# Kernel tuning notes

Hardware: AMD Instinct MI355X
Metric: run time of the kernel (lower is better)

Reference implementation:

```python
import jax, jax.numpy as jnp
import numpy as np

H_IN, W_IN = 128, 128  # sensor grid; region=(1,1), stride=(1,1) -> one RF per pixel


def setup_inputs() -> dict:
    key = jax.random.key(0)
    k1, k2, k3, k4, k5, k6 = jax.random.split(key, 6)
    B, N, C, HID = 8, 2048, 16, 128
    s = 1.0 / np.sqrt(HID)
    features = jax.random.normal(k1, (B, N, C), dtype=jnp.float32)
    coords = jax.random.randint(k2, (B, N, 2), 0, 128, dtype=jnp.int32)  # (x, y)
    w_ih = jax.random.normal(k3, (4 * HID, C), dtype=jnp.float32) * s
    w_hh = jax.random.normal(k4, (4 * HID, HID), dtype=jnp.float32) * s
    b_ih = jax.random.normal(k5, (4 * HID,), dtype=jnp.float32) * s
    b_hh = jax.random.normal(k6, (4 * HID,), dtype=jnp.float32) * s
    return {"features": features, "coords": coords, "w_ih": w_ih,
            "w_hh": w_hh, "b_ih": b_ih, "b_hh": b_hh}


def reference(features, coords, w_ih, w_hh, b_ih, b_hh):
    """MatrixLSTM with 1x1 non-overlapping receptive fields.

    Events (time-ordered along axis 1) are routed to their pixel's RF; a shared
    LSTM is run over each RF's event sequence and the last output per RF is
    scattered into a dense [B, hidden, H, W] map (zeros where no events).
    Implemented as one lax.scan over events with per-RF (h, c) state.
    """
    B, N, C = features.shape
    HID = w_hh.shape[1]
    # coord2idx: raster order y * W + x  -> RF id per event, [B, N]
    rf = coords[:, :, 1].astype(jnp.int32) * W_IN + coords[:, :, 0].astype(jnp.int32)
    bidx = jnp.arange(B)
    bias = b_ih + b_hh

    def step(carry, inp):
        h_all, c_all = carry              # [B, num_rf, HID] each
        x_t, rf_t = inp                   # [B, C], [B]
        h_prev = h_all[bidx, rf_t]        # gather per-RF state, [B, HID]
        c_prev = c_all[bidx, rf_t]
        gates = x_t @ w_ih.T + h_prev @ w_hh.T + bias  # [B, 4*HID]
        i, f, g, o = jnp.split(gates, 4, axis=-1)       # torch LSTM gate order
        i = jax.nn.sigmoid(i)
        f = jax.nn.sigmoid(f)
        g = jnp.tanh(g)
        o = jax.nn.sigmoid(o)
        c_new = f * c_prev + i * g
        h_new = o * jnp.tanh(c_new)
        h_all = h_all.at[bidx, rf_t].set(h_new)        # scatter back
        c_all = c_all.at[bidx, rf_t].set(c_new)
        return (h_all, c_all), None

    h0 = jnp.zeros((B, H_IN * W_IN, HID), features.dtype)
    c0 = jnp.zeros_like(h0)
    (h_all, _), _ = jax.lax.scan(step, (h0, c0),
                                 (features.transpose(1, 0, 2), rf.T))
    # final h per RF == LSTM output at each RF's last event; zeros if no events
    return h_all.reshape(B, H_IN, W_IN, HID).transpose(0, 3, 1, 2)
```

## Files before the change

kernel.cpp:

```cpp
#include <hip/hip_runtime.h>
#include <hip/hip_bf16.h>
#include <math.h>

#define B 8
#define N 2048
#define C 16
#define HID 128
#define NRF 16384
#define MAXLEN 8
#define MAXCH 2048

__device__ __forceinline__ float sigf(float x) { return 1.f / (1.f + expf(-x)); }

__global__ __launch_bounds__(1024) void k_pre(
    const int* __restrict__ coords, const float* __restrict__ w_ih,
    const float* __restrict__ w_hh, const float* __restrict__ b_ih,
    const float* __restrict__ b_hh, float* __restrict__ w_ih_T,
    float* __restrict__ w_hh_T, float* __restrict__ biassum,
    int* __restrict__ map, int* __restrict__ cnt, int* __restrict__ chainrf,
    int* __restrict__ chainlen, int* __restrict__ slots,
    int* __restrict__ m2cnt, int* __restrict__ mlist2) {
    int tid = threadIdx.x;
    if (blockIdx.x < 8) {
        int bb = blockIdx.x;
        __shared__ int cnt_l[NRF];
        __shared__ int nch_l, nmul_l;
#pragma unroll
        for (int i = 0; i < 16; i++) cnt_l[tid + 1024 * i] = 0;
        if (tid == 0) { nch_l = 0; nmul_l = 0; }
#pragma unroll
        for (int i = 0; i < 16; i++) map[bb * NRF + tid + 1024 * i] = -1;
        __syncthreads();
        int n0 = tid, n1 = tid + 1024;
        int2 c0 = ((const int2*)coords)[bb * N + n0];
        int2 c1 = ((const int2*)coords)[bb * N + n1];
        int rf0 = c0.y * 128 + c0.x;
        int rf1 = c1.y * 128 + c1.x;
        int pos0 = atomicAdd(&cnt_l[rf0], 1);
        int pos1 = atomicAdd(&cnt_l[rf1], 1);
        if (pos0 < MAXLEN) slots[((size_t)bb * NRF + rf0) * MAXLEN + pos0] = n0;
        if (pos1 < MAXLEN) slots[((size_t)bb * NRF + rf1) * MAXLEN + pos1] = n1;
        __syncthreads();
#pragma unroll
        for (int e = 0; e < 2; e++) {
            int rf = e ? rf1 : rf0;
            int pos = e ? pos1 : pos0;
            if (pos == 0) {
                int j = atomicAdd(&nch_l, 1);
                int len = cnt_l[rf];
                if (len > MAXLEN) len = MAXLEN;
                chainrf[bb * MAXCH + j] = rf;
                chainlen[bb * MAXCH + j] = len;
                map[bb * NRF + rf] = j;
                if (len >= 2) {
                    int m = atomicAdd(&nmul_l, 1);
                    if (m < 256) mlist2[bb * 256 + m] = bb * MAXCH + j;
                }
            }
        }
        __syncthreads();
        if (tid == 0) {
            cnt[bb] = nch_l;
            m2cnt[bb * 16] = (nmul_l > 256) ? 256 : nmul_l;
        }
    } else {
        int i = (blockIdx.x - 8) * 1024 + tid;
        if (i < C * 512) {
            int c = i >> 9, j = i & 511;
            w_ih_T[i] = w_ih[j * C + c];
        }
        if (i < HID * 512) {
            int k = i >> 9, j = i & 511;
            w_hh_T[i] = w_hh[j * HID + k];
        }
        if (i < 512) biassum[i] = b_ih[i] + b_hh[i];
    }
}

__global__ __launch_bounds__(256) void k_phase0(
    const float* __restrict__ features, const float* __restrict__ w_ih_T,
    const float* __restrict__ biassum, const int* __restrict__ cnt,
    const int* __restrict__ chainrf, const int* __restrict__ chainlen,
    int* __restrict__ slots, float* __restrict__ hfin,
    float* __restrict__ cfin) {
    int tid = threadIdx.x;
    int bb = blockIdx.x >> 8;
    int slot0 = (blockIdx.x & 255) * 8;
    __shared__ float ls_w[C * 512];
    __shared__ float ls_b[512];
    __shared__ int l_idx[8], l_len[8], l_ev0[8];
    int nc = cnt[bb];
    if (tid < 8) {
        int j = slot0 + tid;
        int idx = bb * MAXCH + j;
        if (j < nc) {
            int len = chainlen[idx];
            int* sl = slots + ((size_t)bb * NRF + chainrf[idx]) * MAXLEN;
            int ev0;
            if (len >= 2) {
                int ev[MAXLEN];
#pragma unroll
                for (int t = 0; t < MAXLEN; t++) {
                    int v = sl[t];
                    ev[t] = (t < len) ? v : 0x7fffffff;
                }
#pragma unroll
                for (int a = 0; a < MAXLEN; a++)
#pragma unroll
                    for (int q = 0; q < MAXLEN - 1; q++) {
                        int u = ev[q], v = ev[q + 1];
                        ev[q] = min(u, v);
                        ev[q + 1] = max(u, v);
                    }
                for (int t = 0; t < len; t++) sl[t] = ev[t];
                ev0 = ev[0];
            } else {
                ev0 = sl[0];
            }
            l_idx[tid] = idx; l_len[tid] = len; l_ev0[tid] = ev0;
        } else {
            l_idx[tid] = -1;
        }
    }
    for (int i = tid; i < C * 512; i += 256) ls_w[i] = w_ih_T[i];
    ls_b[tid] = biassum[tid];
    ls_b[tid + 256] = biassum[tid + 256];
    __syncthreads();
    int w = tid >> 6, lane = tid & 63;
#pragma unroll
    for (int s2 = 0; s2 < 2; s2++) {
        int s = 2 * w + s2;
        int idx = l_idx[s];
        if (idx < 0) continue;
        int len = l_len[s];
        int n = l_ev0[s];
        float f = 0.f;
        if (lane < 16) f = features[((size_t)(bb * N + n)) * C + lane];
        float ai0 = ls_b[lane],       ai1 = ls_b[lane + 64];
        float ag0 = ls_b[lane + 256], ag1 = ls_b[lane + 320];
        float ao0 = ls_b[lane + 384], ao1 = ls_b[lane + 448];
#pragma unroll
        for (int c2 = 0; c2 < 16; c2++) {
            float xv = __shfl(f, c2, 64);
            ai0 += ls_w[c2 * 512 + lane]       * xv;
            ai1 += ls_w[c2 * 512 + lane + 64]  * xv;
            ag0 += ls_w[c2 * 512 + lane + 256] * xv;
            ag1 += ls_w[c2 * 512 + lane + 320] * xv;
            ao0 += ls_w[c2 * 512 + lane + 384] * xv;
            ao1 += ls_w[c2 * 512 + lane + 448] * xv;
        }
        float c0 = sigf(ai0) * tanhf(ag0);
        float c1 = sigf(ai1) * tanhf(ag1);
        float h0 = sigf(ao0) * tanhf(c0);
        float h1 = sigf(ao1) * tanhf(c1);
        hfin[(size_t)idx * HID + lane] = h0;
        hfin[(size_t)idx * HID + lane + 64] = h1;
        if (len >= 2) {
            cfin[(size_t)idx * HID + lane] = c0;
            cfin[(size_t)idx * HID + lane + 64] = c1;
        }
    }
}

__global__ __launch_bounds__(512) void k_recur(
    const float* __restrict__ features, const float* __restrict__ w_ih_T,
    const float* __restrict__ w_hh_T, const float* __restrict__ biassum,
    const int* __restrict__ chainrf, const int* __restrict__ chainlen,
    const int* __restrict__ slots, const int* __restrict__ m2cnt,
    const int* __restrict__ mlist2, float* __restrict__ hfin,
    const float* __restrict__ cfin) {
    int tid = threadIdx.x;
    int bb = blockIdx.x >> 7;
    int j0 = blockIdx.x & 127;
    int Mb = m2cnt[bb * 16];
    if (j0 >= Mb) return;
    __shared__ float h_s[HID];
    __shared__ float x_s[16];
    __shared__ float g_s[512];
    float wi[16];
#pragma unroll
    for (int c2 = 0; c2 < 16; c2++) wi[c2] = w_ih_T[c2 * 512 + tid];
    float bsum = biassum[tid];
    for (int j = j0; j < Mb; j += 128) {
        int idx = mlist2[bb * 256 + j];
        int len = chainlen[idx];
        const int* sl = slots + ((size_t)bb * NRF + chainrf[idx]) * MAXLEN;
        if (tid < 128) h_s[tid] = hfin[(size_t)idx * HID + tid];
        float c = (tid < 128) ? cfin[(size_t)idx * HID + tid] : 0.f;
        __syncthreads();
        for (int t = 1; t < len; t++) {
            int n = sl[t];
            if (tid < 16) x_s[tid] = features[((size_t)(bb * N + n)) * C + tid];
            __syncthreads();
            float a0 = bsum, a1 = 0.f, a2 = 0.f, a3 = 0.f;
#pragma unroll
            for (int c2 = 0; c2 < 16; c2++) a0 += wi[c2] * x_s[c2];
#pragma unroll 8
            for (int k = 0; k < 128; k += 4) {
                a0 += w_hh_T[k * 512 + tid] * h_s[k];
                a1 += w_hh_T[(k + 1) * 512 + tid] * h_s[k + 1];
                a2 += w_hh_T[(k + 2) * 512 + tid] * h_s[k + 2];
                a3 += w_hh_T[(k + 3) * 512 + tid] * h_s[k + 3];
            }
            g_s[tid] = (a0 + a1) + (a2 + a3);
            __syncthreads();
            if (tid < 128) {
                float ig = sigf(g_s[tid]);
                float fg = sigf(g_s[tid + 128]);
                float gg = tanhf(g_s[tid + 256]);
                float og = sigf(g_s[tid + 384]);
                c = fg * c + ig * gg;
                h_s[tid] = og * tanhf(c);
            }
            __syncthreads();
        }
        if (tid < 128) hfin[(size_t)idx * HID + tid] = h_s[tid];
        __syncthreads();
    }
}

__global__ __launch_bounds__(256) void k_scatter(
    const float* __restrict__ hfin, const int* __restrict__ map,
    float* __restrict__ out) {
    int b = blockIdx.x >> 7;
    int y = blockIdx.x & 127;
    int t = threadIdx.x;
    int xq = t & 31;
    int hg = t >> 5;
    const int4* mrow = (const int4*)(map + b * NRF + y * 128);
    int4 kk = mrow[xq];
    const float* hb = hfin + (size_t)b * MAXCH * HID;
#pragma unroll
    for (int hh = 0; hh < 16; hh++) {
        int hid = hg * 16 + hh;
        float4 v;
        v.x = (kk.x < 0) ? 0.f : hb[kk.x * HID + hid];
        v.y = (kk.y < 0) ? 0.f : hb[kk.y * HID + hid];
        v.z = (kk.z < 0) ? 0.f : hb[kk.z * HID + hid];
        v.w = (kk.w < 0) ? 0.f : hb[kk.w * HID + hid];
        *(float4*)(out + ((((size_t)b * HID + hid) * 128 + y) * 128) + xq * 4) = v;
    }
}

extern "C" void kernel_launch(void* const* d_in, const int* in_sizes, int n_in,
                              void* d_out, int out_size, void* d_ws, size_t ws_size,
                              hipStream_t stream) {
    const float* features = (const float*)d_in[0];
    const int*   coords   = (const int*)d_in[1];
    const float* w_ih     = (const float*)d_in[2];
    const float* w_hh     = (const float*)d_in[3];
    const float* b_ih     = (const float*)d_in[4];
    const float* b_hh     = (const float*)d_in[5];
    float* out = (float*)d_out;

    char* ws = (char*)d_ws;
    float* w_ih_T   = (float*)(ws + 0);
    float* w_hh_T   = (float*)(ws + 32768);
    float* biassum  = (float*)(ws + 294912);
    int*   map      = (int*)(ws + 296960);
    int*   cnt      = (int*)(ws + 821248);
    int*   chainrf  = (int*)(ws + 821312);
    int*   chainlen = (int*)(ws + 886848);
    int*   slots    = (int*)(ws + 952384);
    float* hfin     = (float*)(ws + 5146688);
    float* cfin     = (float*)(ws + 13535296);
    int*   m2cnt    = (int*)(ws + 21923904);
    int*   mlist2   = (int*)(ws + 21924416);

    k_pre<<<dim3(81), dim3(1024), 0, stream>>>(
        coords, w_ih, w_hh, b_ih, b_hh, w_ih_T, w_hh_T, biassum,
        map, cnt, chainrf, chainlen, slots, m2cnt, mlist2);
    k_phase0<<<dim3(2048), dim3(256), 0, stream>>>(
        features, w_ih_T, biassum, cnt, chainrf, chainlen, slots, hfin, cfin);
    k_recur<<<dim3(B * 128), dim3(512), 0, stream>>>(
        features, w_ih_T, w_hh_T, biassum, chainrf, chainlen, slots,
        m2cnt, mlist2, hfin, cfin);
    k_scatter<<<dim3(B * 128), dim3(256), 0, stream>>>(hfin, map, out);
}
```

Before: 132.9 us.

## Fuse recurrence into first-step kernel, keeping chain state in shared memory

Merges the separate recurrence kernel into the first-step kernel. Each block now runs the remaining LSTM steps for its own multi-event chains, with h and c held in shared memory, so the cfin round trip, the mlist2 compaction and one kernel launch are no longer needed. The trade-off is serialisation inside a block: 256 threads loop over up to 8 chains in turn, each thread computing two gates per step. Blocks that have long chains may also take longer than the rest.

```diff
diff --git a/kernel.cpp b/kernel.cpp
--- a/kernel.cpp
+++ b/kernel.cpp
@@ -18,16 +18,15 @@
     const float* __restrict__ b_hh, float* __restrict__ w_ih_T,
     float* __restrict__ w_hh_T, float* __restrict__ biassum,
     int* __restrict__ map, int* __restrict__ cnt, int* __restrict__ chainrf,
-    int* __restrict__ chainlen, int* __restrict__ slots,
-    int* __restrict__ m2cnt, int* __restrict__ mlist2) {
+    int* __restrict__ chainlen, int* __restrict__ slots) {
     int tid = threadIdx.x;
     if (blockIdx.x < 8) {
         int bb = blockIdx.x;
         __shared__ int cnt_l[NRF];
-        __shared__ int nch_l, nmul_l;
+        __shared__ int nch_l;
 #pragma unroll
         for (int i = 0; i < 16; i++) cnt_l[tid + 1024 * i] = 0;
-        if (tid == 0) { nch_l = 0; nmul_l = 0; }
+        if (tid == 0) nch_l = 0;
 #pragma unroll
         for (int i = 0; i < 16; i++) map[bb * NRF + tid + 1024 * i] = -1;
         __syncthreads();
@@ -52,17 +51,10 @@
                 chainrf[bb * MAXCH + j] = rf;
                 chainlen[bb * MAXCH + j] = len;
                 map[bb * NRF + rf] = j;
-                if (len >= 2) {
-                    int m = atomicAdd(&nmul_l, 1);
-                    if (m < 256) mlist2[bb * 256 + m] = bb * MAXCH + j;
-                }
-            }
-        }
-        __syncthreads();
-        if (tid == 0) {
-            cnt[bb] = nch_l;
-            m2cnt[bb * 16] = (nmul_l > 256) ? 256 : nmul_l;
-        }
+            }
+        }
+        __syncthreads();
+        if (tid == 0) cnt[bb] = nch_l;
     } else {
         int i = (blockIdx.x - 8) * 1024 + tid;
         if (i < C * 512) {
@@ -77,17 +69,20 @@
     }
 }
 
-__global__ __launch_bounds__(256) void k_phase0(
+__global__ __launch_bounds__(256) void k_phase(
     const float* __restrict__ features, const float* __restrict__ w_ih_T,
-    const float* __restrict__ biassum, const int* __restrict__ cnt,
-    const int* __restrict__ chainrf, const int* __restrict__ chainlen,
-    int* __restrict__ slots, float* __restrict__ hfin,
-    float* __restrict__ cfin) {
+    const float* __restrict__ w_hh_T, const float* __restrict__ biassum,
+    const int* __restrict__ cnt, const int* __restrict__ chainrf,
+    const int* __restrict__ chainlen, int* __restrict__ slots,
+    float* __restrict__ hfin) {
     int tid = threadIdx.x;
     int bb = blockIdx.x >> 8;
     int slot0 = (blockIdx.x & 255) * 8;
     __shared__ float ls_w[C * 512];
     __shared__ float ls_b[512];
+    __shared__ float h_st[8][HID], c_st[8][HID];
+    __shared__ float g_s[512];
+    __shared__ float x_s[16];
     __shared__ int l_idx[8], l_len[8], l_ev0[8];
     int nc = cnt[bb];
     if (tid < 8) {
@@ -119,10 +114,11 @@
             }
             l_idx[tid] = idx; l_len[tid] = len; l_ev0[tid] = ev0;
         } else {
-            l_idx[tid] = -1;
-        }
-    }
-    for (int i = tid; i < C * 512; i += 256) ls_w[i] = w_ih_T[i];
+            l_idx[tid] = -1; l_len[tid] = 0;
+        }
+    }
+    for (int i = tid; i < C * 128; i += 256)
+        ((float4*)ls_w)[i] = ((const float4*)w_ih_T)[i];
     ls_b[tid] = biassum[tid];
     ls_b[tid + 256] = biassum[tid + 256];
     __syncthreads();
@@ -153,69 +149,52 @@
         float c1 = sigf(ai1) * tanhf(ag1);
         float h0 = sigf(ao0) * tanhf(c0);
         float h1 = sigf(ao1) * tanhf(c1);
-        hfin[(size_t)idx * HID + lane] = h0;
-        hfin[(size_t)idx * HID + lane + 64] = h1;
-        if (len >= 2) {
-            cfin[(size_t)idx * HID + lane] = c0;
-            cfin[(size_t)idx * HID + lane + 64] = c1;
-        }
-    }
-}
-
-__global__ __launch_bounds__(512) void k_recur(
-    const float* __restrict__ features, const float* __restrict__ w_ih_T,
-    const float* __restrict__ w_hh_T, const float* __restrict__ biassum,
-    const int* __restrict__ chainrf, const int* __restrict__ chainlen,
-    const int* __restrict__ slots, const int* __restrict__ m2cnt,
-    const int* __restrict__ mlist2, float* __restrict__ hfin,
-    const float* __restrict__ cfin) {
-    int tid = threadIdx.x;
-    int bb = blockIdx.x >> 7;
-    int j0 = blockIdx.x & 127;
-    int Mb = m2cnt[bb * 16];
-    if (j0 >= Mb) return;
-    __shared__ float h_s[HID];
-    __shared__ float x_s[16];
-    __shared__ float g_s[512];
-    float wi[16];
-#pragma unroll
-    for (int c2 = 0; c2 < 16; c2++) wi[c2] = w_ih_T[c2 * 512 + tid];
-    float bsum = biassum[tid];
-    for (int j = j0; j < Mb; j += 128) {
-        int idx = mlist2[bb * 256 + j];
-        int len = chainlen[idx];
+        if (len == 1) {
+            hfin[(size_t)idx * HID + lane] = h0;
+            hfin[(size_t)idx * HID + lane + 64] = h1;
+        } else {
+            h_st[s][lane] = h0; h_st[s][lane + 64] = h1;
+            c_st[s][lane] = c0; c_st[s][lane + 64] = c1;
+        }
+    }
+    for (int s = 0; s < 8; s++) {
+        int len = l_len[s];
+        if (len < 2) continue;
+        int idx = l_idx[s];
         const int* sl = slots + ((size_t)bb * NRF + chainrf[idx]) * MAXLEN;
-        if (tid < 128) h_s[tid] = hfin[(size_t)idx * HID + tid];
-        float c = (tid < 128) ? cfin[(size_t)idx * HID + tid] : 0.f;
-        __syncthreads();
         for (int t = 1; t < len; t++) {
-            int n = sl[t];
-            if (tid < 16) x_s[tid] = features[((size_t)(bb * N + n)) * C + tid];
             __syncthreads();
-            float a0 = bsum, a1 = 0.f, a2 = 0.f, a3 = 0.f;
-#pragma unroll
-            for (int c2 = 0; c2 < 16; c2++) a0 += wi[c2] * x_s[c2];
+            if (tid < 16)
+                x_s[tid] = features[((size_t)(bb * N + sl[t])) * C + tid];
+            __syncthreads();
+            float a0 = ls_b[tid], a1 = ls_b[tid + 256];
+#pragma unroll
+            for (int c2 = 0; c2 < 16; c2++) {
+                float xv = x_s[c2];
+                a0 += ls_w[c2 * 512 + tid] * xv;
+                a1 += ls_w[c2 * 512 + tid + 256] * xv;
+            }
 #pragma unroll 8
-            for (int k = 0; k < 128; k += 4) {
-                a0 += w_hh_T[k * 512 + tid] * h_s[k];
-                a1 += w_hh_T[(k + 1) * 512 + tid] * h_s[k + 1];
-                a2 += w_hh_T[(k + 2) * 512 + tid] * h_s[k + 2];
-                a3 += w_hh_T[(k + 3) * 512 + tid] * h_s[k + 3];
-            }
-            g_s[tid] = (a0 + a1) + (a2 + a3);
+            for (int k = 0; k < 128; k++) {
+                float hv = h_st[s][k];
+                a0 += w_hh_T[k * 512 + tid] * hv;
+                a1 += w_hh_T[k * 512 + tid + 256] * hv;
+            }
+            g_s[tid] = a0;
+            g_s[tid + 256] = a1;
             __syncthreads();
             if (tid < 128) {
                 float ig = sigf(g_s[tid]);
                 float fg = sigf(g_s[tid + 128]);
                 float gg = tanhf(g_s[tid + 256]);
                 float og = sigf(g_s[tid + 384]);
-                c = fg * c + ig * gg;
-                h_s[tid] = og * tanhf(c);
-            }
-            __syncthreads();
-        }
-        if (tid < 128) hfin[(size_t)idx * HID + tid] = h_s[tid];
-        __syncthreads();
+                float cn = fg * c_st[s][tid] + ig * gg;
+                c_st[s][tid] = cn;
+                h_st[s][tid] = og * tanhf(cn);
+            }
+        }
+        __syncthreads();
+        if (tid < 128) hfin[(size_t)idx * HID + tid] = h_st[s][tid];
     }
 }
 
@@ -263,17 +242,11 @@
     int*   chainlen = (int*)(ws + 886848);
     int*   slots    = (int*)(ws + 952384);
     float* hfin     = (float*)(ws + 5146688);
-    float* cfin     = (float*)(ws + 13535296);
-    int*   m2cnt    = (int*)(ws + 21923904);
-    int*   mlist2   = (int*)(ws + 21924416);
 
     k_pre<<<dim3(81), dim3(1024), 0, stream>>>(
         coords, w_ih, w_hh, b_ih, b_hh, w_ih_T, w_hh_T, biassum,
-        map, cnt, chainrf, chainlen, slots, m2cnt, mlist2);
-    k_phase0<<<dim3(2048), dim3(256), 0, stream>>>(
-        features, w_ih_T, biassum, cnt, chainrf, chainlen, slots, hfin, cfin);
-    k_recur<<<dim3(B * 128), dim3(512), 0, stream>>>(
-        features, w_ih_T, w_hh_T, biassum, chainrf, chainlen, slots,
-        m2cnt, mlist2, hfin, cfin);
+        map, cnt, chainrf, chainlen, slots);
+    k_phase<<<dim3(2048), dim3(256), 0, stream>>>(
+        features, w_ih_T, w_hh_T, biassum, cnt, chainrf, chainlen, slots, hfin);
     k_scatter<<<dim3(B * 128), dim3(256), 0, stream>>>(hfin, map, out);
 }
```

After: 139.5 us. 5.0% more time.
